# Performance work log

Measured on AMD Instinct MI355X. Metric: run time of the kernel, lower is better.

Reference implementation:

```python
import jax, jax.numpy as jnp
import numpy as np

B, T, C = 4, 2048, 1024
N_HEAD = 16
HEAD_DIM = C // N_HEAD


def setup_inputs() -> dict:
    key = jax.random.key(0)
    k1, k2, k3 = jax.random.split(key, 3)
    scale = 1.0 / np.sqrt(C)
    return {
        "x": jax.random.normal(k1, (B, T, C), dtype=jnp.float32),
        "W_attn": jax.random.normal(k2, (C, 3 * C), dtype=jnp.float32) * scale,
        "b_attn": jnp.zeros((3 * C,), dtype=jnp.float32),
        "W_proj": jax.random.normal(k3, (C, C), dtype=jnp.float32) * scale,
        "b_proj": jnp.zeros((C,), dtype=jnp.float32),
    }


def reference(x, W_attn, b_attn, W_proj, b_proj):
    Bt, Tt, Ct = x.shape
    qkv = x @ W_attn + b_attn                      # [B,T,3C]
    q, k, v = jnp.split(qkv, 3, axis=-1)
    # [B,T,C] -> [B,H,T,D]
    def heads(t):
        return t.reshape(Bt, Tt, N_HEAD, HEAD_DIM).transpose(0, 2, 1, 3)
    q, k, v = heads(q), heads(k), heads(v)
    att = jnp.einsum("bhqd,bhkd->bhqk", q, k) * (1.0 / np.sqrt(HEAD_DIM))
    causal = jnp.tril(jnp.ones((Tt, Tt), dtype=bool))
    att = jnp.where(causal, att, jnp.finfo(att.dtype).min)
    att = jax.nn.softmax(att, axis=-1)
    # dropout = 0.0 (eval mode): identity
    y = jnp.einsum("bhqk,bhkd->bhqd", att, v)      # [B,H,T,D]
    y = y.transpose(0, 2, 1, 3).reshape(Bt, Tt, Ct)
    return y @ W_proj + b_proj
```

## Files before the change

kernel.cpp:

```cpp
#include <hip/hip_runtime.h>
#include <hip/hip_bf16.h>
#include <cstdint>

#define B_SZ 4
#define T_SZ 2048
#define C_SZ 1024
#define H_SZ 16
#define D_SZ 64
#define BT_SZ (B_SZ * T_SZ)
#define C3_SZ (3 * C_SZ)
#define NKC (C_SZ / 32)
#define NKT (C_SZ / 64)

typedef __attribute__((ext_vector_type(8))) short bf16x8;
typedef __attribute__((ext_vector_type(4))) float f32x4;
typedef __attribute__((ext_vector_type(4))) unsigned short ushort4v;
typedef __attribute__((ext_vector_type(4))) unsigned int uint4v;

typedef __attribute__((address_space(3))) unsigned int lds_u32;
typedef __attribute__((address_space(1))) const unsigned int glb_u32;

__device__ __forceinline__ unsigned short f2bf(float f) {
  unsigned u = __builtin_bit_cast(unsigned, f);
  u += 0x7fffu + ((u >> 16) & 1u);
  return (unsigned short)(u >> 16);
}

__device__ __forceinline__ unsigned packbf2(float lo, float hi) {
  return __builtin_amdgcn_perm(__builtin_bit_cast(unsigned, hi),
                               __builtin_bit_cast(unsigned, lo), 0x07060302u);
}

__device__ __forceinline__ void gll16(const unsigned short* g,
                                      unsigned short* l) {
  __builtin_amdgcn_global_load_lds((glb_u32*)g, (lds_u32*)l, 16, 0, 0);
}


__device__ __forceinline__ void pack_x_task(const float* __restrict__ x,
                                            unsigned short* __restrict__ Af,
                                            int task, int lane) {
  const int quad = lane >> 4, n = lane & 15;
  const int tb = task >> 5, kc = task & 31;
  const float* src = x + (size_t)(tb * 16 + n) * C_SZ + kc * 32 + quad * 8;
  float4 a = *(const float4*)src;
  float4 b = *(const float4*)(src + 4);
  ushort4v o0, o1;
  o0[0] = f2bf(a.x); o0[1] = f2bf(a.y); o0[2] = f2bf(a.z); o0[3] = f2bf(a.w);
  o1[0] = f2bf(b.x); o1[1] = f2bf(b.y); o1[2] = f2bf(b.z); o1[3] = f2bf(b.w);
  unsigned short* dst = Af + ((size_t)((tb * NKC + kc) * 4 + quad) * 16 + n) * 8;
  *(ushort4v*)dst = o0;
  *(ushort4v*)(dst + 4) = o1;
}

__device__ __forceinline__ void pack_w_task(const float* __restrict__ W,
                                            unsigned short* __restrict__ Wb,
                                            int N, int task, int lane) {
  const int quad = lane >> 4, n = lane & 15;
  const int nt = task >> 5, kc = task & 31;
  const int col = nt * 16 + n;
  const int k0 = kc * 32 + quad * 8;
  ushort4v o0, o1;
#pragma unroll
  for (int i = 0; i < 4; ++i) o0[i] = f2bf(W[(size_t)(k0 + i) * N + col]);
#pragma unroll
  for (int i = 0; i < 4; ++i) o1[i] = f2bf(W[(size_t)(k0 + 4 + i) * N + col]);
  unsigned short* dst = Wb + ((size_t)((nt * NKC + kc) * 4 + quad) * 16 + n) * 8;
  *(ushort4v*)dst = o0;
  *(ushort4v*)(dst + 4) = o1;
}

__global__ __launch_bounds__(256) void pack_all(
    const float* __restrict__ x, const float* __restrict__ Wa,
    const float* __restrict__ Wp, unsigned short* __restrict__ Af,
    unsigned short* __restrict__ Wab, unsigned short* __restrict__ Wpb) {
  const int bx = blockIdx.x;
  const int sub = threadIdx.x >> 6;
  const int lane = threadIdx.x & 63;
  if (bx < 4096) {
    pack_x_task(x, Af, bx * 4 + sub, lane);
  } else if (bx < 4096 + 1536) {
    pack_w_task(Wa, Wab, C3_SZ, (bx - 4096) * 4 + sub, lane);
  } else {
    pack_w_task(Wp, Wpb, C_SZ, (bx - 5632) * 4 + sub, lane);
  }
}

__device__ __forceinline__ void gemm_8ph_mainloop(
    const unsigned short* __restrict__ A, const unsigned short* __restrict__ B,
    int tbB, int ntB, unsigned short* smem, f32x4 acc[4][4]) {
  const int tid = threadIdx.x;
  const int w = tid >> 6, lane = tid & 63;
  const int quad = lane >> 4, n = lane & 15;
  const int wr = w >> 2, wc = w & 3;

  auto stageA = [&](int buf, int t, int h) {
    gll16(A + ((size_t)(tbB + h * 4 + (w >> 1)) * NKC + t * 2 + (w & 1)) * 512 +
              lane * 8,
          smem + buf * 24576 + ((h * 4 + (w >> 1)) * 2 + (w & 1)) * 512);
  };
  auto stageB = [&](int buf, int t, int h) {
    const unsigned short* src =
        B + ((size_t)(ntB + h * 8 + w) * NKC + t * 2) * 512 + lane * 8;
    unsigned short* dst = smem + buf * 24576 + 8192 + (h * 8 + w) * 1024;
    gll16(src, dst);
    gll16(src + 512, dst + 512);
  };

  auto ldA = [&](int buf, int mh, bf16x8 af[2][2]) {
#pragma unroll
    for (int mi = 0; mi < 2; ++mi)
#pragma unroll
      for (int kc = 0; kc < 2; ++kc)
        af[mi][kc] = *(const bf16x8*)(smem + buf * 24576 +
            ((wr * 4 + mh * 2 + mi) * 2 + kc) * 512 + quad * 128 + n * 8);
  };
  auto ldB = [&](int buf, bf16x8 bfr[4][2]) {
#pragma unroll
    for (int nn = 0; nn < 4; ++nn)
#pragma unroll
      for (int kc = 0; kc < 2; ++kc)
        bfr[nn][kc] = *(const bf16x8*)(smem + buf * 24576 + 8192 +
            ((wc * 4 + nn) * 2 + kc) * 512 + quad * 128 + n * 8);
  };
  auto mmaQ = [&](int mh, int nh, bf16x8 af[2][2], bf16x8 bfr[4][2]) {
    __builtin_amdgcn_s_setprio(1);
#pragma unroll
    for (int mi = 0; mi < 2; ++mi)
#pragma unroll
      for (int nj = 0; nj < 2; ++nj)
#pragma unroll
        for (int kc = 0; kc < 2; ++kc)
          acc[mh * 2 + mi][nh * 2 + nj] =
              __builtin_amdgcn_mfma_f32_16x16x32_bf16(
                  af[mi][kc], bfr[nh * 2 + nj][kc],
                  acc[mh * 2 + mi][nh * 2 + nj], 0, 0, 0);
    __builtin_amdgcn_s_setprio(0);
  };

  stageB(0, 0, 0); stageB(0, 0, 1); stageA(0, 0, 0); stageA(0, 0, 1);
  stageB(1, 1, 0); stageB(1, 1, 1); stageA(1, 1, 0);
  asm volatile("s_waitcnt vmcnt(5)" ::: "memory");
  __builtin_amdgcn_s_barrier();

  auto tileStep = [&](int t, int cur, bool s1, bool s2) {
    const int nxt = cur ^ 1;
    bf16x8 af[2][2], bfr[4][2];
    ldA(cur, 0, af);
    ldB(cur, bfr);
    if (s1) stageA(nxt, t + 1, 1);
    __builtin_amdgcn_s_barrier();
    mmaQ(0, 0, af, bfr);
    __builtin_amdgcn_s_barrier();
    if (s2) stageB(cur, t + 2, 0);
    __builtin_amdgcn_s_barrier();
    mmaQ(0, 1, af, bfr);
    __builtin_amdgcn_s_barrier();
    ldA(cur, 1, af);
    if (s2) stageB(cur, t + 2, 1);
    __builtin_amdgcn_s_barrier();
    mmaQ(1, 1, af, bfr);
    __builtin_amdgcn_s_barrier();
    if (s2) stageA(cur, t + 2, 0);
    __builtin_amdgcn_s_barrier();
    mmaQ(1, 0, af, bfr);
    if (s2) {
      asm volatile("s_waitcnt vmcnt(5)" ::: "memory");
    } else if (s1) {
      asm volatile("s_waitcnt vmcnt(0)" ::: "memory");
    }
    __builtin_amdgcn_s_barrier();
  };

  for (int t = 0; t < NKT - 2; ++t) tileStep(t, t & 1, true, true);
  tileStep(NKT - 2, (NKT - 2) & 1, true, false);
  tileStep(NKT - 1, (NKT - 1) & 1, false, false);
}

__global__ __launch_bounds__(512) void qkv_mfma(
    const unsigned short* __restrict__ Af, const unsigned short* __restrict__ Wab,
    const float* __restrict__ bias, unsigned short* __restrict__ Qf,
    unsigned short* __restrict__ Kf, unsigned short* __restrict__ Vf) {
  __shared__ __align__(16) unsigned short smem[49152];
  const int tid = threadIdx.x;
  const int w = tid >> 6, lane = tid & 63;
  const int quad = lane >> 4, n = lane & 15;
  const int wr = w >> 2, wc = w & 3;
  const int f = blockIdx.x;
  const int xcd = f & 7, i = f >> 3;
  const int by = xcd * 8 + (i / 12);
  const int bx = i % 12;
  f32x4 acc[4][4];
#pragma unroll
  for (int m = 0; m < 4; ++m)
#pragma unroll
    for (int nn = 0; nn < 4; ++nn) acc[m][nn] = (f32x4){0.f, 0.f, 0.f, 0.f};

  gemm_8ph_mainloop(Af, Wab, by * 8, bx * 16, smem, acc);

  const int cb = bx * 256 + wc * 64;
  const int which = cb >> 10;
  const int h = (cb & 1023) >> 6;
  const int gr0 = by * 128 + wr * 64;
  const int b = gr0 >> 11;
  const int t0 = gr0 & 2047;
  const size_t bhoff = (size_t)(b * H_SZ + h) * (T_SZ * D_SZ);
  float bfl[4];
#pragma unroll
  for (int nn = 0; nn < 4; ++nn) bfl[nn] = bias[cb + nn * 16 + n];

  if (which < 2) {
    unsigned short* dst = ((which == 0) ? Qf : Kf) + bhoff;
    const float scl = (which == 0) ? 0.18033688f : 1.0f;
#pragma unroll
    for (int m = 0; m < 4; ++m) {
      const int tb = (t0 + m * 16) >> 4;
#pragma unroll
      for (int nn = 0; nn < 4; ++nn) {
        const int dc = nn >> 1;
        const int qd = (nn & 1) * 2 + (n >> 3);
        const int jq = n & 7;
#pragma unroll
        for (int r = 0; r < 4; ++r) {
          const int nq = quad * 4 + r;
          dst[((size_t)((tb * 2 + dc) * 4 + qd)) * 128 + nq * 8 + jq] =
              f2bf((acc[m][nn][r] + bfl[nn]) * scl);
        }
      }
    }
  } else {
    unsigned short* dst = Vf + bhoff;
    const int gb0 = t0 >> 5;
#pragma unroll
    for (int m = 0; m < 4; ++m) {
      const int gb = gb0 + (m >> 1);
#pragma unroll
      for (int nn = 0; nn < 4; ++nn) {
#pragma unroll
        for (int r = 0; r < 4; ++r) {
          dst[((size_t)((gb * 4 + nn) * 4 + quad)) * 128 + n * 8 + (m & 1) * 4 + r] =
              f2bf(acc[m][nn][r] + bfl[nn]);
        }
      }
    }
  }
}

__global__ __launch_bounds__(512) void proj_mfma(
    const unsigned short* __restrict__ Yf, const unsigned short* __restrict__ Wpb,
    const float* __restrict__ bias, float* __restrict__ out) {
  __shared__ __align__(16) unsigned short smem[49152];
  const int tid = threadIdx.x;
  const int w = tid >> 6, lane = tid & 63;
  const int quad = lane >> 4, n = lane & 15;
  const int wr = w >> 2, wc = w & 3;
  const int f = blockIdx.x;
  const int xcd = f & 7, i = f >> 3;
  const int by = xcd * 8 + (i / 4);
  const int bx = i % 4;
  f32x4 acc[4][4];
#pragma unroll
  for (int m = 0; m < 4; ++m)
#pragma unroll
    for (int nn = 0; nn < 4; ++nn) acc[m][nn] = (f32x4){0.f, 0.f, 0.f, 0.f};

  gemm_8ph_mainloop(Yf, Wpb, by * 8, bx * 16, smem, acc);

  const int cb = bx * 256 + wc * 64;
  const int gr0 = by * 128 + wr * 64;
  float bfl[4];
#pragma unroll
  for (int nn = 0; nn < 4; ++nn) bfl[nn] = bias[cb + nn * 16 + n];
#pragma unroll
  for (int m = 0; m < 4; ++m)
#pragma unroll
    for (int nn = 0; nn < 4; ++nn)
#pragma unroll
      for (int r = 0; r < 4; ++r)
        out[(size_t)(gr0 + m * 16 + quad * 4 + r) * C_SZ + cb + nn * 16 + n] =
            acc[m][nn][r] + bfl[nn];
}

__global__ __launch_bounds__(64) void attn_mfma(
    const unsigned short* __restrict__ Qf,
    const unsigned short* __restrict__ Kf,
    const unsigned short* __restrict__ Vf, unsigned short* __restrict__ Yf) {
  const int lane = threadIdx.x;
  const int quad = lane >> 4;
  const int n = lane & 15;
  const int bx = blockIdx.x;
  const int qt = 31 - (bx >> 6);
  const int bh = bx & 63;
  const int b = bh >> 4, h = bh & 15;
  const int wq0 = qt * 64;
  const size_t bhoff = (size_t)bh * (T_SZ * D_SZ);
  const bf16x8* Qp = (const bf16x8*)(Qf + bhoff);
  const bf16x8* Kp = (const bf16x8*)(Kf + bhoff);
  const bf16x8* Vp = (const bf16x8*)(Vf + bhoff);

  bf16x8 qfr[4][2];
#pragma unroll
  for (int m = 0; m < 4; ++m) {
    const int tb = (wq0 >> 4) + m;
#pragma unroll
    for (int dc = 0; dc < 2; ++dc)
      qfr[m][dc] = Qp[((tb * 2 + dc) * 4 + quad) * 16 + n];
  }

  bf16x8 kfr[4][2], vfr[2][4];
  f32x4 O[4][4];
  f32x4 ls[4];
#pragma unroll
  for (int m = 0; m < 4; ++m) {
    ls[m] = (f32x4){0.f, 0.f, 0.f, 0.f};
#pragma unroll
    for (int dv = 0; dv < 4; ++dv) O[m][dv] = (f32x4){0.f, 0.f, 0.f, 0.f};
  }

#pragma unroll
  for (int s = 0; s < 4; ++s) {
    kfr[s][0] = Kp[((s * 2 + 0) * 4 + quad) * 16 + n];
    kfr[s][1] = Kp[((s * 2 + 1) * 4 + quad) * 16 + n];
  }
#pragma unroll
  for (int g = 0; g < 2; ++g)
#pragma unroll
    for (int dv = 0; dv < 4; ++dv)
      vfr[g][dv] = Vp[((g * 4 + dv) * 4 + quad) * 16 + n];

  for (int kt = 0; kt < qt; ++kt) {
#pragma unroll
    for (int m = 0; m < 4; ++m) {
      f32x4 st[4];
#pragma unroll
      for (int s = 0; s < 4; ++s) {
        f32x4 z = {0.f, 0.f, 0.f, 0.f};
        z = __builtin_amdgcn_mfma_f32_16x16x32_bf16(kfr[s][0], qfr[m][0], z, 0, 0, 0);
        z = __builtin_amdgcn_mfma_f32_16x16x32_bf16(kfr[s][1], qfr[m][1], z, 0, 0, 0);
        st[s] = z;
      }
      if (m == 3) {
        const int tb0 = (kt + 1) * 4;
#pragma unroll
        for (int s = 0; s < 4; ++s) {
          kfr[s][0] = Kp[(((tb0 + s) * 2 + 0) * 4 + quad) * 16 + n];
          kfr[s][1] = Kp[(((tb0 + s) * 2 + 1) * 4 + quad) * 16 + n];
        }
      }
      uint4v pw[2];
#pragma unroll
      for (int s = 0; s < 4; ++s) {
        float pr[4];
#pragma unroll
        for (int r = 0; r < 4; ++r) {
          pr[r] = __builtin_amdgcn_exp2f(st[s][r]);
          ls[m][r] += pr[r];
        }
        pw[s >> 1][(s & 1) * 2 + 0] = packbf2(pr[0], pr[1]);
        pw[s >> 1][(s & 1) * 2 + 1] = packbf2(pr[2], pr[3]);
      }
#pragma unroll
      for (int g = 0; g < 2; ++g) {
        const bf16x8 pg = __builtin_bit_cast(bf16x8, pw[g]);
#pragma unroll
        for (int dv = 0; dv < 4; ++dv)
          O[m][dv] = __builtin_amdgcn_mfma_f32_16x16x32_bf16(
              pg, vfr[g][dv], O[m][dv], 0, 0, 0);
      }
      if (m == 3) {
        const int gb0 = (kt + 1) * 2;
#pragma unroll
        for (int g = 0; g < 2; ++g)
#pragma unroll
          for (int dv = 0; dv < 4; ++dv)
            vfr[g][dv] = Vp[(((gb0 + g) * 4 + dv) * 4 + quad) * 16 + n];
      }
    }
  }

  {
#pragma unroll
    for (int m = 0; m < 4; ++m) {
      f32x4 st[4];
#pragma unroll
      for (int s = 0; s < 4; ++s) {
        f32x4 z = {0.f, 0.f, 0.f, 0.f};
        if (s <= m) {
          z = __builtin_amdgcn_mfma_f32_16x16x32_bf16(kfr[s][0], qfr[m][0], z, 0, 0, 0);
          z = __builtin_amdgcn_mfma_f32_16x16x32_bf16(kfr[s][1], qfr[m][1], z, 0, 0, 0);
        }
        st[s] = z;
      }
      uint4v pw[2] = {(uint4v){0, 0, 0, 0}, (uint4v){0, 0, 0, 0}};
#pragma unroll
      for (int s = 0; s < 4; ++s) {
        if (s <= m) {
          float pr[4];
#pragma unroll
          for (int r = 0; r < 4; ++r) {
            float v = st[s][r];
            if (s == m && quad * 4 + r > n) v = -1e30f;
            pr[r] = __builtin_amdgcn_exp2f(v);
            ls[m][r] += pr[r];
          }
          pw[s >> 1][(s & 1) * 2 + 0] = packbf2(pr[0], pr[1]);
          pw[s >> 1][(s & 1) * 2 + 1] = packbf2(pr[2], pr[3]);
        }
      }
#pragma unroll
      for (int g = 0; g < 2; ++g) {
        if (g * 2 <= m) {
          const bf16x8 pg = __builtin_bit_cast(bf16x8, pw[g]);
#pragma unroll
          for (int dv = 0; dv < 4; ++dv)
            O[m][dv] = __builtin_amdgcn_mfma_f32_16x16x32_bf16(
                pg, vfr[g][dv], O[m][dv], 0, 0, 0);
        }
      }
    }
  }

#pragma unroll
  for (int m = 0; m < 4; ++m) {
    float lt = ls[m][0] + ls[m][1] + ls[m][2] + ls[m][3];
    lt += __shfl_xor(lt, 16);
    lt += __shfl_xor(lt, 32);
    const float inv = 1.0f / lt;
    float iv[4];
#pragma unroll
    for (int r = 0; r < 4; ++r) iv[r] = __shfl(inv, quad * 4 + r);
    const int tb = (b * T_SZ + wq0 + m * 16) >> 4;
#pragma unroll
    for (int dv = 0; dv < 4; ++dv) {
      const int kc = h * 2 + (dv >> 1);
      const int qa = (dv & 1) * 2 + (n >> 3);
      const int ja = n & 7;
#pragma unroll
      for (int r = 0; r < 4; ++r) {
        const int na = quad * 4 + r;
        Yf[((size_t)((tb * NKC + kc) * 4 + qa)) * 128 + na * 8 + ja] =
            f2bf(O[m][dv][r] * iv[r]);
      }
    }
  }
}

extern "C" void kernel_launch(void* const* d_in, const int* in_sizes, int n_in,
                              void* d_out, int out_size, void* d_ws,
                              size_t ws_size, hipStream_t stream) {
  const float* x = (const float*)d_in[0];
  const float* W_attn = (const float*)d_in[1];
  const float* b_attn = (const float*)d_in[2];
  const float* W_proj = (const float*)d_in[3];
  const float* b_proj = (const float*)d_in[4];
  float* out = (float*)d_out;

  const size_t perbf = (size_t)B_SZ * H_SZ * T_SZ * D_SZ;
  unsigned short* Af = (unsigned short*)d_ws;
  unsigned short* Wab = Af + (size_t)BT_SZ * C_SZ;
  unsigned short* Wpb = Wab + (size_t)C_SZ * C3_SZ;
  unsigned short* Qf = Wpb + (size_t)C_SZ * C_SZ;
  unsigned short* Kf = Qf + perbf;
  unsigned short* Vf = Kf + perbf;
  unsigned short* Yf = Vf + perbf;

  pack_all<<<6144, 256, 0, stream>>>(x, W_attn, W_proj, Af, Wab, Wpb);
  qkv_mfma<<<768, 512, 0, stream>>>(Af, Wab, b_attn, Qf, Kf, Vf);
  attn_mfma<<<dim3(32 * B_SZ * H_SZ), 64, 0, stream>>>(Qf, Kf, Vf, Yf);
  proj_mfma<<<256, 512, 0, stream>>>(Yf, Wpb, b_proj, out);
}
```

Baseline: 224.7 us.

## Enlarge GEMM block tile to 256x256 with 8x4 accumulators per wave

Doubles the M dimension of the QKV and projection GEMM block tiles from 128 to 256 rows. Each wave now holds 8x4 accumulator fragments, the LDS buffers grow to 64K elements, and the staging and fragment-load schedule is restructured to match, with an explicit lgkmcnt wait before each MFMA group. The aim is more arithmetic per byte loaded and fewer global loads. The cost is half as many blocks (384 and 128) on a 256-CU part, which risks poor occupancy and wave quantization, plus higher register pressure.

```diff
diff --git a/kernel.cpp b/kernel.cpp
--- a/kernel.cpp
+++ b/kernel.cpp
@@ -86,93 +86,97 @@
   }
 }
 
-__device__ __forceinline__ void gemm_8ph_mainloop(
+__device__ __forceinline__ void gemm_m201_mainloop(
     const unsigned short* __restrict__ A, const unsigned short* __restrict__ B,
-    int tbB, int ntB, unsigned short* smem, f32x4 acc[4][4]) {
+    int tbB, int ntB, unsigned short* smem, f32x4 acc[8][4]) {
   const int tid = threadIdx.x;
   const int w = tid >> 6, lane = tid & 63;
   const int quad = lane >> 4, n = lane & 15;
   const int wr = w >> 2, wc = w & 3;
 
   auto stageA = [&](int buf, int t, int h) {
-    gll16(A + ((size_t)(tbB + h * 4 + (w >> 1)) * NKC + t * 2 + (w & 1)) * 512 +
-              lane * 8,
-          smem + buf * 24576 + ((h * 4 + (w >> 1)) * 2 + (w & 1)) * 512);
+    const int tb = 4 * h + (w & 3) + 8 * (w >> 2);
+#pragma unroll
+    for (int kc = 0; kc < 2; ++kc)
+      gll16(A + ((size_t)(tbB + tb) * NKC + t * 2 + kc) * 512 + lane * 8,
+            smem + buf * 32768 + (tb * 2 + kc) * 512);
   };
   auto stageB = [&](int buf, int t, int h) {
-    const unsigned short* src =
-        B + ((size_t)(ntB + h * 8 + w) * NKC + t * 2) * 512 + lane * 8;
-    unsigned short* dst = smem + buf * 24576 + 8192 + (h * 8 + w) * 1024;
-    gll16(src, dst);
-    gll16(src + 512, dst + 512);
-  };
-
-  auto ldA = [&](int buf, int mh, bf16x8 af[2][2]) {
-#pragma unroll
-    for (int mi = 0; mi < 2; ++mi)
+    const int nt = (w >> 1) * 4 + 2 * h + (w & 1);
+#pragma unroll
+    for (int kc = 0; kc < 2; ++kc)
+      gll16(B + ((size_t)(ntB + nt) * NKC + t * 2 + kc) * 512 + lane * 8,
+            smem + buf * 32768 + 16384 + (nt * 2 + kc) * 512);
+  };
+
+  auto ldA = [&](int buf, int mh, bf16x8 af[4][2]) {
+#pragma unroll
+    for (int mi = 0; mi < 4; ++mi)
 #pragma unroll
       for (int kc = 0; kc < 2; ++kc)
-        af[mi][kc] = *(const bf16x8*)(smem + buf * 24576 +
-            ((wr * 4 + mh * 2 + mi) * 2 + kc) * 512 + quad * 128 + n * 8);
-  };
-  auto ldB = [&](int buf, bf16x8 bfr[4][2]) {
-#pragma unroll
-    for (int nn = 0; nn < 4; ++nn)
+        af[mi][kc] = *(const bf16x8*)(smem + buf * 32768 +
+            ((wr * 8 + mh * 4 + mi) * 2 + kc) * 512 + quad * 128 + n * 8);
+  };
+  auto ldB = [&](int buf, int nh, bf16x8 bfr[2][2]) {
+#pragma unroll
+    for (int nj = 0; nj < 2; ++nj)
 #pragma unroll
       for (int kc = 0; kc < 2; ++kc)
-        bfr[nn][kc] = *(const bf16x8*)(smem + buf * 24576 + 8192 +
-            ((wc * 4 + nn) * 2 + kc) * 512 + quad * 128 + n * 8);
-  };
-  auto mmaQ = [&](int mh, int nh, bf16x8 af[2][2], bf16x8 bfr[4][2]) {
+        bfr[nj][kc] = *(const bf16x8*)(smem + buf * 32768 + 16384 +
+            ((wc * 4 + nh * 2 + nj) * 2 + kc) * 512 + quad * 128 + n * 8);
+  };
+  auto mmaQ = [&](int mh, int nh, bf16x8 af[4][2], bf16x8 bfr[2][2]) {
+    asm volatile("s_waitcnt lgkmcnt(0)");
     __builtin_amdgcn_s_setprio(1);
 #pragma unroll
-    for (int mi = 0; mi < 2; ++mi)
+    for (int mi = 0; mi < 4; ++mi)
 #pragma unroll
       for (int nj = 0; nj < 2; ++nj)
 #pragma unroll
         for (int kc = 0; kc < 2; ++kc)
-          acc[mh * 2 + mi][nh * 2 + nj] =
+          acc[mh * 4 + mi][nh * 2 + nj] =
               __builtin_amdgcn_mfma_f32_16x16x32_bf16(
-                  af[mi][kc], bfr[nh * 2 + nj][kc],
-                  acc[mh * 2 + mi][nh * 2 + nj], 0, 0, 0);
+                  af[mi][kc], bfr[nj][kc], acc[mh * 4 + mi][nh * 2 + nj],
+                  0, 0, 0);
     __builtin_amdgcn_s_setprio(0);
   };
 
-  stageB(0, 0, 0); stageB(0, 0, 1); stageA(0, 0, 0); stageA(0, 0, 1);
-  stageB(1, 1, 0); stageB(1, 1, 1); stageA(1, 1, 0);
-  asm volatile("s_waitcnt vmcnt(5)" ::: "memory");
+  stageA(0, 0, 0); stageA(0, 0, 1); stageB(0, 0, 0); stageB(0, 0, 1);
+  stageA(1, 1, 0); stageB(1, 1, 0); stageB(1, 1, 1);
+  asm volatile("s_waitcnt vmcnt(6)" ::: "memory");
   __builtin_amdgcn_s_barrier();
 
-  auto tileStep = [&](int t, int cur, bool s1, bool s2) {
+  auto tileStep = [&](int s, int cur, bool s1, bool s2) {
     const int nxt = cur ^ 1;
-    bf16x8 af[2][2], bfr[4][2];
+    bf16x8 af[4][2], bf0[2][2], bf1[2][2];
     ldA(cur, 0, af);
-    ldB(cur, bfr);
-    if (s1) stageA(nxt, t + 1, 1);
-    __builtin_amdgcn_s_barrier();
-    mmaQ(0, 0, af, bfr);
-    __builtin_amdgcn_s_barrier();
-    if (s2) stageB(cur, t + 2, 0);
-    __builtin_amdgcn_s_barrier();
-    mmaQ(0, 1, af, bfr);
+    ldB(cur, 0, bf0);
+    if (s1) stageA(nxt, s + 1, 1);
+    __builtin_amdgcn_s_barrier();
+    mmaQ(0, 0, af, bf0);
+    __builtin_amdgcn_s_barrier();
+    ldB(cur, 1, bf1);
+    if (s2) stageA(cur, s + 2, 0);
+    __builtin_amdgcn_s_barrier();
+    mmaQ(0, 1, af, bf1);
     __builtin_amdgcn_s_barrier();
     ldA(cur, 1, af);
-    if (s2) stageB(cur, t + 2, 1);
-    __builtin_amdgcn_s_barrier();
-    mmaQ(1, 1, af, bfr);
-    __builtin_amdgcn_s_barrier();
-    if (s2) stageA(cur, t + 2, 0);
-    __builtin_amdgcn_s_barrier();
-    mmaQ(1, 0, af, bfr);
+    if (s2) stageB(cur, s + 2, 0);
+    __builtin_amdgcn_s_barrier();
+    mmaQ(1, 1, af, bf1);
+    __builtin_amdgcn_s_barrier();
+    if (s2) stageB(cur, s + 2, 1);
+    __builtin_amdgcn_s_barrier();
+    mmaQ(1, 0, af, bf0);
     if (s2) {
-      asm volatile("s_waitcnt vmcnt(5)" ::: "memory");
+      asm volatile("s_waitcnt vmcnt(6)" ::: "memory");
     } else if (s1) {
       asm volatile("s_waitcnt vmcnt(0)" ::: "memory");
     }
     __builtin_amdgcn_s_barrier();
   };
 
-  for (int t = 0; t < NKT - 2; ++t) tileStep(t, t & 1, true, true);
+  for (int s = 0; s < NKT - 2; ++s) tileStep(s, s & 1, true, true);
   tileStep(NKT - 2, (NKT - 2) & 1, true, false);
   tileStep(NKT - 1, (NKT - 1) & 1, false, false);
 }
@@ -181,27 +185,27 @@
     const unsigned short* __restrict__ Af, const unsigned short* __restrict__ Wab,
     const float* __restrict__ bias, unsigned short* __restrict__ Qf,
     unsigned short* __restrict__ Kf, unsigned short* __restrict__ Vf) {
-  __shared__ __align__(16) unsigned short smem[49152];
+  __shared__ __align__(16) unsigned short smem[65536];
   const int tid = threadIdx.x;
   const int w = tid >> 6, lane = tid & 63;
   const int quad = lane >> 4, n = lane & 15;
   const int wr = w >> 2, wc = w & 3;
   const int f = blockIdx.x;
   const int xcd = f & 7, i = f >> 3;
-  const int by = xcd * 8 + (i / 12);
+  const int by = xcd * 4 + (i / 12);
   const int bx = i % 12;
-  f32x4 acc[4][4];
-#pragma unroll
-  for (int m = 0; m < 4; ++m)
+  f32x4 acc[8][4];
+#pragma unroll
+  for (int m = 0; m < 8; ++m)
 #pragma unroll
     for (int nn = 0; nn < 4; ++nn) acc[m][nn] = (f32x4){0.f, 0.f, 0.f, 0.f};
 
-  gemm_8ph_mainloop(Af, Wab, by * 8, bx * 16, smem, acc);
+  gemm_m201_mainloop(Af, Wab, by * 16, bx * 16, smem, acc);
 
   const int cb = bx * 256 + wc * 64;
   const int which = cb >> 10;
   const int h = (cb & 1023) >> 6;
-  const int gr0 = by * 128 + wr * 64;
+  const int gr0 = by * 256 + wr * 128;
   const int b = gr0 >> 11;
   const int t0 = gr0 & 2047;
   const size_t bhoff = (size_t)(b * H_SZ + h) * (T_SZ * D_SZ);
@@ -213,7 +217,7 @@
     unsigned short* dst = ((which == 0) ? Qf : Kf) + bhoff;
     const float scl = (which == 0) ? 0.18033688f : 1.0f;
 #pragma unroll
-    for (int m = 0; m < 4; ++m) {
+    for (int m = 0; m < 8; ++m) {
       const int tb = (t0 + m * 16) >> 4;
 #pragma unroll
       for (int nn = 0; nn < 4; ++nn) {
@@ -232,7 +236,7 @@
     unsigned short* dst = Vf + bhoff;
     const int gb0 = t0 >> 5;
 #pragma unroll
-    for (int m = 0; m < 4; ++m) {
+    for (int m = 0; m < 8; ++m) {
       const int gb = gb0 + (m >> 1);
 #pragma unroll
       for (int nn = 0; nn < 4; ++nn) {
@@ -249,30 +253,30 @@
 __global__ __launch_bounds__(512) void proj_mfma(
     const unsigned short* __restrict__ Yf, const unsigned short* __restrict__ Wpb,
     const float* __restrict__ bias, float* __restrict__ out) {
-  __shared__ __align__(16) unsigned short smem[49152];
+  __shared__ __align__(16) unsigned short smem[65536];
   const int tid = threadIdx.x;
   const int w = tid >> 6, lane = tid & 63;
   const int quad = lane >> 4, n = lane & 15;
   const int wr = w >> 2, wc = w & 3;
   const int f = blockIdx.x;
   const int xcd = f & 7, i = f >> 3;
-  const int by = xcd * 8 + (i / 4);
+  const int by = xcd * 4 + (i / 4);
   const int bx = i % 4;
-  f32x4 acc[4][4];
-#pragma unroll
-  for (int m = 0; m < 4; ++m)
+  f32x4 acc[8][4];
+#pragma unroll
+  for (int m = 0; m < 8; ++m)
 #pragma unroll
     for (int nn = 0; nn < 4; ++nn) acc[m][nn] = (f32x4){0.f, 0.f, 0.f, 0.f};
 
-  gemm_8ph_mainloop(Yf, Wpb, by * 8, bx * 16, smem, acc);
+  gemm_m201_mainloop(Yf, Wpb, by * 16, bx * 16, smem, acc);
 
   const int cb = bx * 256 + wc * 64;
-  const int gr0 = by * 128 + wr * 64;
+  const int gr0 = by * 256 + wr * 128;
   float bfl[4];
 #pragma unroll
   for (int nn = 0; nn < 4; ++nn) bfl[nn] = bias[cb + nn * 16 + n];
 #pragma unroll
-  for (int m = 0; m < 4; ++m)
+  for (int m = 0; m < 8; ++m)
 #pragma unroll
     for (int nn = 0; nn < 4; ++nn)
 #pragma unroll
@@ -465,7 +469,7 @@
   unsigned short* Yf = Vf + perbf;
 
   pack_all<<<6144, 256, 0, stream>>>(x, W_attn, W_proj, Af, Wab, Wpb);
-  qkv_mfma<<<768, 512, 0, stream>>>(Af, Wab, b_attn, Qf, Kf, Vf);
+  qkv_mfma<<<384, 512, 0, stream>>>(Af, Wab, b_attn, Qf, Kf, Vf);
   attn_mfma<<<dim3(32 * B_SZ * H_SZ), 64, 0, stream>>>(Qf, Kf, Vf, Yf);
-  proj_mfma<<<256, 512, 0, stream>>>(Yf, Wpb, b_proj, out);
-}
+  proj_mfma<<<128, 512, 0, stream>>>(Yf, Wpb, b_proj, out);
+}
```

Result: slower. 239.4 us (+6.5%).
